# Kernel tuning notes

Measured on AMD Instinct MI355X. Metric: run time of the kernel, lower is better.

## Reference

```python
import jax, jax.numpy as jnp
import numpy as np

B, L, D, C = 32, 2048, 1024, 1024  # batch, max_length, input_size, context_size


def setup_inputs() -> dict:
    key = jax.random.key(0)
    ks = jax.random.split(key, 4)
    sequence = jax.random.normal(ks[0], (B, L, D), dtype=jnp.float32)
    query = jax.random.normal(ks[1], (B, C), dtype=jnp.float32)
    # lengths in [1, L] so every row has at least one unmasked position
    lengths = jax.random.randint(ks[2], (B,), 1, L + 1, dtype=jnp.int32)
    W_h = jax.random.normal(ks[3], (C, D), dtype=jnp.float32) / np.sqrt(D).astype(np.float32)
    b_h = jnp.zeros((C,), dtype=jnp.float32)
    return {"sequence": sequence, "query": query, "lengths": lengths, "W_h": W_h, "b_h": b_h}


def reference(sequence, query, lengths, W_h, b_h):
    # method='general': energies = (W_h @ sequence + b_h) . query
    h = jnp.einsum('bld,cd->blc', sequence, W_h) + b_h          # [B, L, C]
    energies = jnp.einsum('blc,bc->bl', h, query)                # [B, L]
    # sequence_mask(lengths, L): True where position < length
    mask = jnp.arange(energies.shape[1]) < lengths[:, None]      # [B, L]
    # masked_normalization_inf: fill masked positions with -inf, softmax
    masked = jnp.where(mask, energies, -jnp.inf)
    scores = jax.nn.softmax(masked, axis=-1)                     # [B, L]
    contexts = jnp.einsum('bl,bld->bd', scores, sequence)        # [B, D]
    return contexts, scores
```

## Files before the change

### kernel.cpp

```cpp
#include <hip/hip_runtime.h>
#include <math.h>

#define B_ 32
#define L_ 2048
#define D_ 1024
#define C_ 1024
#define WROWS 8
#define BROWS 32
#define NCH (L_ / BROWS)


__global__ __launch_bounds__(256) void k_vpart(const float* __restrict__ q,
                                               const float* __restrict__ W,
                                               float* __restrict__ vpart) {
    int cc = blockIdx.x, dc = blockIdx.y;
    int t  = threadIdx.x;
    __shared__ float qs[B_][65];
    #pragma unroll
    for (int i = 0; i < 8; ++i) {
        int idx = t + i * 256;
        int b = idx >> 6, cl = idx & 63;
        qs[b][cl] = q[b * C_ + cc * 64 + cl];
    }
    __syncthreads();

    int dl4 = t & 15;
    int bg  = t >> 4;
    float4 a0 = {0,0,0,0}, a1 = {0,0,0,0};
    const float4* W4 = reinterpret_cast<const float4*>(W);
    for (int c = 0; c < 64; ++c) {
        float4 w = W4[(size_t)(cc * 64 + c) * (D_ / 4) + dc * 16 + dl4];
        float q0 = qs[bg * 2 + 0][c];
        float q1 = qs[bg * 2 + 1][c];
        a0.x = fmaf(q0, w.x, a0.x); a0.y = fmaf(q0, w.y, a0.y);
        a0.z = fmaf(q0, w.z, a0.z); a0.w = fmaf(q0, w.w, a0.w);
        a1.x = fmaf(q1, w.x, a1.x); a1.y = fmaf(q1, w.y, a1.y);
        a1.z = fmaf(q1, w.z, a1.z); a1.w = fmaf(q1, w.w, a1.w);
    }
    size_t base = ((size_t)cc * B_ + bg * 2) * D_ + dc * 64 + dl4 * 4;
    *reinterpret_cast<float4*>(vpart + base)       = a0;
    *reinterpret_cast<float4*>(vpart + base + D_)  = a1;
}

__global__ __launch_bounds__(256) void k_vreduce(const float* __restrict__ vpart,
                                                 float* __restrict__ v,
                                                 const float* __restrict__ q,
                                                 const float* __restrict__ bh,
                                                 float* __restrict__ cb) {
    int b = blockIdx.x, dq = blockIdx.y, t = threadIdx.x;
    int d = dq * 256 + t;
    float a = 0.f;
    #pragma unroll
    for (int cc = 0; cc < 16; ++cc)
        a += vpart[((size_t)cc * B_ + b) * D_ + d];
    v[(size_t)b * D_ + d] = a;

    if (dq == 0) {
        float s = 0.f;
        for (int c = t; c < C_; c += 256) s += bh[c] * q[b * C_ + c];
        __shared__ float red[256];
        red[t] = s; __syncthreads();
        for (int off = 128; off > 0; off >>= 1) {
            if (t < off) red[t] += red[t + off];
            __syncthreads();
        }
        if (t == 0) cb[b] = red[0];
    }
}

__global__ __launch_bounds__(256) void k_fused(const float* __restrict__ seq,
                                               const float* __restrict__ v,
                                               const float* __restrict__ cb,
                                               const int* __restrict__ lenp,
                                               float* __restrict__ energ,
                                               float* __restrict__ pm,
                                               float* __restrict__ ps,
                                               float* __restrict__ pc) {
    int b  = blockIdx.y;
    int ch = blockIdx.x;
    int len = lenp[b];
    int l0 = ch * BROWS;
    if (l0 >= len) return;
    int wid = threadIdx.x >> 6, lane = threadIdx.x & 63;
    int t = threadIdx.x;
    int lw0 = l0 + wid * WROWS;

    const float* vb = v + (size_t)b * D_;
    float4 v0 = *reinterpret_cast<const float4*>(vb +       lane * 4);
    float4 v1 = *reinterpret_cast<const float4*>(vb + 256 + lane * 4);
    float4 v2 = *reinterpret_cast<const float4*>(vb + 512 + lane * 4);
    float4 v3 = *reinterpret_cast<const float4*>(vb + 768 + lane * 4);
    float cbb = cb[b];

    float m = -INFINITY, s = 0.f;
    float c[16];
    #pragma unroll
    for (int i = 0; i < 16; ++i) c[i] = 0.f;

    __shared__ float e_sm[BROWS];
    __shared__ float lm[4], ls[4];
    __shared__ float lc[4][D_];

    if (lw0 < len) {
        #pragma unroll
        for (int r = 0; r < WROWS; ++r) {
            int l = lw0 + r;
            bool valid = l < len;
            const float* row = seq + ((size_t)b * L_ + l) * D_;
            float4 s0 = *reinterpret_cast<const float4*>(row +       lane * 4);
            float4 s1 = *reinterpret_cast<const float4*>(row + 256 + lane * 4);
            float4 s2 = *reinterpret_cast<const float4*>(row + 512 + lane * 4);
            float4 s3 = *reinterpret_cast<const float4*>(row + 768 + lane * 4);
            float acc = 0.f;
            acc = fmaf(s0.x, v0.x, acc); acc = fmaf(s0.y, v0.y, acc);
            acc = fmaf(s0.z, v0.z, acc); acc = fmaf(s0.w, v0.w, acc);
            acc = fmaf(s1.x, v1.x, acc); acc = fmaf(s1.y, v1.y, acc);
            acc = fmaf(s1.z, v1.z, acc); acc = fmaf(s1.w, v1.w, acc);
            acc = fmaf(s2.x, v2.x, acc); acc = fmaf(s2.y, v2.y, acc);
            acc = fmaf(s2.z, v2.z, acc); acc = fmaf(s2.w, v2.w, acc);
            acc = fmaf(s3.x, v3.x, acc); acc = fmaf(s3.y, v3.y, acc);
            acc = fmaf(s3.z, v3.z, acc); acc = fmaf(s3.w, v3.w, acc);
            #pragma unroll
            for (int off = 32; off; off >>= 1) acc += __shfl_xor(acc, off);
            float e = acc + cbb;
            if (lane == 0) e_sm[wid * WROWS + r] = e;
            float mnew  = valid ? fmaxf(m, e) : m;
            float scale = (m == mnew) ? 1.f : __expf(m - mnew);
            float p     = valid ? __expf(e - mnew) : 0.f;
            s = s * scale + p;
            c[ 0] = fmaf(p, s0.x, c[ 0] * scale); c[ 1] = fmaf(p, s0.y, c[ 1] * scale);
            c[ 2] = fmaf(p, s0.z, c[ 2] * scale); c[ 3] = fmaf(p, s0.w, c[ 3] * scale);
            c[ 4] = fmaf(p, s1.x, c[ 4] * scale); c[ 5] = fmaf(p, s1.y, c[ 5] * scale);
            c[ 6] = fmaf(p, s1.z, c[ 6] * scale); c[ 7] = fmaf(p, s1.w, c[ 7] * scale);
            c[ 8] = fmaf(p, s2.x, c[ 8] * scale); c[ 9] = fmaf(p, s2.y, c[ 9] * scale);
            c[10] = fmaf(p, s2.z, c[10] * scale); c[11] = fmaf(p, s2.w, c[11] * scale);
            c[12] = fmaf(p, s3.x, c[12] * scale); c[13] = fmaf(p, s3.y, c[13] * scale);
            c[14] = fmaf(p, s3.z, c[14] * scale); c[15] = fmaf(p, s3.w, c[15] * scale);
            m = mnew;
        }
    }

    {
        float4 w0 = {c[ 0], c[ 1], c[ 2], c[ 3]};
        float4 w1 = {c[ 4], c[ 5], c[ 6], c[ 7]};
        float4 w2 = {c[ 8], c[ 9], c[10], c[11]};
        float4 w3 = {c[12], c[13], c[14], c[15]};
        *reinterpret_cast<float4*>(&lc[wid][      lane * 4]) = w0;
        *reinterpret_cast<float4*>(&lc[wid][256 + lane * 4]) = w1;
        *reinterpret_cast<float4*>(&lc[wid][512 + lane * 4]) = w2;
        *reinterpret_cast<float4*>(&lc[wid][768 + lane * 4]) = w3;
        if (lane == 0) { lm[wid] = m; ls[wid] = s; }
    }
    __syncthreads();

    if (t < BROWS) energ[(size_t)b * L_ + l0 + t] = e_sm[t];

    float mb = fmaxf(fmaxf(lm[0], lm[1]), fmaxf(lm[2], lm[3]));
    float w0 = (lm[0] == mb) ? 1.f : __expf(lm[0] - mb);
    float w1 = (lm[1] == mb) ? 1.f : __expf(lm[1] - mb);
    float w2 = (lm[2] == mb) ? 1.f : __expf(lm[2] - mb);
    float w3 = (lm[3] == mb) ? 1.f : __expf(lm[3] - mb);
    float sb = w0 * ls[0] + w1 * ls[1] + w2 * ls[2] + w3 * ls[3];

    float4 a0 = *reinterpret_cast<const float4*>(&lc[0][t * 4]);
    float4 a1 = *reinterpret_cast<const float4*>(&lc[1][t * 4]);
    float4 a2 = *reinterpret_cast<const float4*>(&lc[2][t * 4]);
    float4 a3 = *reinterpret_cast<const float4*>(&lc[3][t * 4]);
    float4 o;
    o.x = w0 * a0.x + w1 * a1.x + w2 * a2.x + w3 * a3.x;
    o.y = w0 * a0.y + w1 * a1.y + w2 * a2.y + w3 * a3.y;
    o.z = w0 * a0.z + w1 * a1.z + w2 * a2.z + w3 * a3.z;
    o.w = w0 * a0.w + w1 * a1.w + w2 * a2.w + w3 * a3.w;

    size_t pidx = (size_t)b * NCH + ch;
    if (t == 0) { pm[pidx] = mb; ps[pidx] = sb; }
    *reinterpret_cast<float4*>(pc + pidx * D_ + t * 4) = o;
}

__global__ __launch_bounds__(256) void k_final(const float* __restrict__ pm,
                                               const float* __restrict__ ps,
                                               const float* __restrict__ pc,
                                               const float* __restrict__ energ,
                                               const int* __restrict__ lenp,
                                               float* __restrict__ ctx,
                                               float* __restrict__ scores) {
    int b = blockIdx.x, sl = blockIdx.y, t = threadIdx.x;
    int len = lenp[b];
    int nch = (len + BROWS - 1) / BROWS;
    __shared__ float wgt[NCH];
    __shared__ float Msh, Ssh;
    if (t < 64) {
        float mi = (t < nch) ? pm[(size_t)b * NCH + t] : -INFINITY;
        float si = (t < nch) ? ps[(size_t)b * NCH + t] : 0.f;
        float M = mi;
        #pragma unroll
        for (int off = 32; off; off >>= 1) M = fmaxf(M, __shfl_xor(M, off));
        float ew = (t < nch) ? __expf(mi - M) : 0.f;
        float S  = ew * si;
        #pragma unroll
        for (int off = 32; off; off >>= 1) S += __shfl_xor(S, off);
        if (t < nch) wgt[t] = ew / S;
        if (t == 0) { Msh = M; Ssh = S; }
    }
    __syncthreads();
    float M = Msh;
    float invS = 1.f / Ssh;

    if (t < 128) {
        int d = sl * 128 + t;
        float o = 0.f;
        for (int ch = 0; ch < nch; ++ch)
            o = fmaf(wgt[ch], pc[((size_t)b * NCH + ch) * D_ + d], o);
        ctx[(size_t)b * D_ + d] = o;
    }

    int l = sl * 256 + t;
    float e = energ[(size_t)b * L_ + l];
    scores[(size_t)b * L_ + l] = (l < len) ? __expf(e - M) * invS : 0.f;
}

extern "C" void kernel_launch(void* const* d_in, const int* in_sizes, int n_in,
                              void* d_out, int out_size, void* d_ws, size_t ws_size,
                              hipStream_t stream) {
    const float* seq     = (const float*)d_in[0];
    const float* query   = (const float*)d_in[1];
    const int*   lengths = (const int*)  d_in[2];
    const float* W_h     = (const float*)d_in[3];
    const float* b_h     = (const float*)d_in[4];

    float* out    = (float*)d_out;
    float* ctx    = out;
    float* scores = out + B_ * D_;

    float* ws    = (float*)d_ws;
    float* v     = ws;
    float* cb    = ws + 32768;
    float* energ = ws + 32800;
    float* vpart = ws + 98336;
    float* pm    = ws + 622624;
    float* ps    = ws + 624672;
    float* pc    = ws + 626720;

    k_vpart  <<<dim3(16, 16), 256, 0, stream>>>(query, W_h, vpart);
    k_vreduce<<<dim3(B_, 4), 256, 0, stream>>>(vpart, v, query, b_h, cb);
    k_fused  <<<dim3(NCH, B_), 256, 0, stream>>>(seq, v, cb, lengths, energ, pm, ps, pc);
    k_final  <<<dim3(B_, 8), 256, 0, stream>>>(pm, ps, pc, energ, lengths, ctx, scores);
}
```

Before: 46.86 us.

## Merge four kernels into two using last-block atomic counters for reductions

```diff
diff --git a/kernel.cpp b/kernel.cpp
--- a/kernel.cpp
+++ b/kernel.cpp
@@ -10,12 +10,17 @@
 #define NCH (L_ / BROWS)
 
 
-__global__ __launch_bounds__(256) void k_vpart(const float* __restrict__ q,
-                                               const float* __restrict__ W,
-                                               float* __restrict__ vpart) {
+__global__ __launch_bounds__(256) void k_prep(const float* __restrict__ q,
+                                              const float* __restrict__ W,
+                                              const float* __restrict__ bh,
+                                              float* __restrict__ vpart,
+                                              float* __restrict__ v,
+                                              float* __restrict__ cb,
+                                              int* __restrict__ cnt) {
     int cc = blockIdx.x, dc = blockIdx.y;
     int t  = threadIdx.x;
     __shared__ float qs[B_][65];
+    __shared__ int lastf;
     #pragma unroll
     for (int i = 0; i < 8; ++i) {
         int idx = t + i * 256;
@@ -38,157 +43,164 @@
         a1.z = fmaf(q1, w.z, a1.z); a1.w = fmaf(q1, w.w, a1.w);
     }
     size_t base = ((size_t)cc * B_ + bg * 2) * D_ + dc * 64 + dl4 * 4;
-    *reinterpret_cast<float4*>(vpart + base)       = a0;
-    *reinterpret_cast<float4*>(vpart + base + D_)  = a1;
+    *reinterpret_cast<float4*>(vpart + base)      = a0;
+    *reinterpret_cast<float4*>(vpart + base + D_) = a1;
+
+    __syncthreads();
+    if (t == 0) {
+        __threadfence();
+        int old = atomicAdd(&cnt[dc], 1);
+        lastf = (old == 15);
+    }
+    __syncthreads();
+    if (!lastf) return;
+    __threadfence();
+
+    #pragma unroll
+    for (int i = 0; i < 8; ++i) {
+        int idx = t + i * 256;
+        int b = idx >> 6, dl = idx & 63;
+        int d = dc * 64 + dl;
+        float a = 0.f;
+        #pragma unroll
+        for (int c2 = 0; c2 < 16; ++c2)
+            a += vpart[((size_t)c2 * B_ + b) * D_ + d];
+        v[(size_t)b * D_ + d] = a;
+    }
+    if (dc == 0) {
+        int b = t >> 3, l8 = t & 7;
+        float s = 0.f;
+        for (int c = l8; c < C_; c += 8) s += bh[c] * q[b * C_ + c];
+        s += __shfl_xor(s, 4); s += __shfl_xor(s, 2); s += __shfl_xor(s, 1);
+        if (l8 == 0) cb[b] = s;
+    }
 }
 
-__global__ __launch_bounds__(256) void k_vreduce(const float* __restrict__ vpart,
-                                                 float* __restrict__ v,
-                                                 const float* __restrict__ q,
-                                                 const float* __restrict__ bh,
-                                                 float* __restrict__ cb) {
-    int b = blockIdx.x, dq = blockIdx.y, t = threadIdx.x;
-    int d = dq * 256 + t;
-    float a = 0.f;
-    #pragma unroll
-    for (int cc = 0; cc < 16; ++cc)
-        a += vpart[((size_t)cc * B_ + b) * D_ + d];
-    v[(size_t)b * D_ + d] = a;
-
-    if (dq == 0) {
-        float s = 0.f;
-        for (int c = t; c < C_; c += 256) s += bh[c] * q[b * C_ + c];
-        __shared__ float red[256];
-        red[t] = s; __syncthreads();
-        for (int off = 128; off > 0; off >>= 1) {
-            if (t < off) red[t] += red[t + off];
-            __syncthreads();
-        }
-        if (t == 0) cb[b] = red[0];
-    }
-}
-
-__global__ __launch_bounds__(256) void k_fused(const float* __restrict__ seq,
-                                               const float* __restrict__ v,
-                                               const float* __restrict__ cb,
-                                               const int* __restrict__ lenp,
-                                               float* __restrict__ energ,
-                                               float* __restrict__ pm,
-                                               float* __restrict__ ps,
-                                               float* __restrict__ pc) {
+__global__ __launch_bounds__(256) void k_mega(const float* __restrict__ seq,
+                                              const float* __restrict__ v,
+                                              const float* __restrict__ cb,
+                                              const int* __restrict__ lenp,
+                                              float* __restrict__ energ,
+                                              float* __restrict__ pm,
+                                              float* __restrict__ ps,
+                                              float* __restrict__ pc,
+                                              int* __restrict__ done,
+                                              float* __restrict__ ctx,
+                                              float* __restrict__ scores) {
     int b  = blockIdx.y;
     int ch = blockIdx.x;
     int len = lenp[b];
     int l0 = ch * BROWS;
-    if (l0 >= len) return;
-    int wid = threadIdx.x >> 6, lane = threadIdx.x & 63;
-    int t = threadIdx.x;
-    int lw0 = l0 + wid * WROWS;
-
-    const float* vb = v + (size_t)b * D_;
-    float4 v0 = *reinterpret_cast<const float4*>(vb +       lane * 4);
-    float4 v1 = *reinterpret_cast<const float4*>(vb + 256 + lane * 4);
-    float4 v2 = *reinterpret_cast<const float4*>(vb + 512 + lane * 4);
-    float4 v3 = *reinterpret_cast<const float4*>(vb + 768 + lane * 4);
-    float cbb = cb[b];
-
-    float m = -INFINITY, s = 0.f;
-    float c[16];
-    #pragma unroll
-    for (int i = 0; i < 16; ++i) c[i] = 0.f;
+    int t = threadIdx.x, wid = t >> 6, lane = t & 63;
 
     __shared__ float e_sm[BROWS];
     __shared__ float lm[4], ls[4];
     __shared__ float lc[4][D_];
-
-    if (lw0 < len) {
-        #pragma unroll
-        for (int r = 0; r < WROWS; ++r) {
-            int l = lw0 + r;
-            bool valid = l < len;
-            const float* row = seq + ((size_t)b * L_ + l) * D_;
-            float4 s0 = *reinterpret_cast<const float4*>(row +       lane * 4);
-            float4 s1 = *reinterpret_cast<const float4*>(row + 256 + lane * 4);
-            float4 s2 = *reinterpret_cast<const float4*>(row + 512 + lane * 4);
-            float4 s3 = *reinterpret_cast<const float4*>(row + 768 + lane * 4);
-            float acc = 0.f;
-            acc = fmaf(s0.x, v0.x, acc); acc = fmaf(s0.y, v0.y, acc);
-            acc = fmaf(s0.z, v0.z, acc); acc = fmaf(s0.w, v0.w, acc);
-            acc = fmaf(s1.x, v1.x, acc); acc = fmaf(s1.y, v1.y, acc);
-            acc = fmaf(s1.z, v1.z, acc); acc = fmaf(s1.w, v1.w, acc);
-            acc = fmaf(s2.x, v2.x, acc); acc = fmaf(s2.y, v2.y, acc);
-            acc = fmaf(s2.z, v2.z, acc); acc = fmaf(s2.w, v2.w, acc);
-            acc = fmaf(s3.x, v3.x, acc); acc = fmaf(s3.y, v3.y, acc);
-            acc = fmaf(s3.z, v3.z, acc); acc = fmaf(s3.w, v3.w, acc);
-            #pragma unroll
-            for (int off = 32; off; off >>= 1) acc += __shfl_xor(acc, off);
-            float e = acc + cbb;
-            if (lane == 0) e_sm[wid * WROWS + r] = e;
-            float mnew  = valid ? fmaxf(m, e) : m;
-            float scale = (m == mnew) ? 1.f : __expf(m - mnew);
-            float p     = valid ? __expf(e - mnew) : 0.f;
-            s = s * scale + p;
-            c[ 0] = fmaf(p, s0.x, c[ 0] * scale); c[ 1] = fmaf(p, s0.y, c[ 1] * scale);
-            c[ 2] = fmaf(p, s0.z, c[ 2] * scale); c[ 3] = fmaf(p, s0.w, c[ 3] * scale);
-            c[ 4] = fmaf(p, s1.x, c[ 4] * scale); c[ 5] = fmaf(p, s1.y, c[ 5] * scale);
-            c[ 6] = fmaf(p, s1.z, c[ 6] * scale); c[ 7] = fmaf(p, s1.w, c[ 7] * scale);
-            c[ 8] = fmaf(p, s2.x, c[ 8] * scale); c[ 9] = fmaf(p, s2.y, c[ 9] * scale);
-            c[10] = fmaf(p, s2.z, c[10] * scale); c[11] = fmaf(p, s2.w, c[11] * scale);
-            c[12] = fmaf(p, s3.x, c[12] * scale); c[13] = fmaf(p, s3.y, c[13] * scale);
-            c[14] = fmaf(p, s3.z, c[14] * scale); c[15] = fmaf(p, s3.w, c[15] * scale);
-            m = mnew;
-        }
-    }
-
-    {
-        float4 w0 = {c[ 0], c[ 1], c[ 2], c[ 3]};
-        float4 w1 = {c[ 4], c[ 5], c[ 6], c[ 7]};
-        float4 w2 = {c[ 8], c[ 9], c[10], c[11]};
-        float4 w3 = {c[12], c[13], c[14], c[15]};
-        *reinterpret_cast<float4*>(&lc[wid][      lane * 4]) = w0;
-        *reinterpret_cast<float4*>(&lc[wid][256 + lane * 4]) = w1;
-        *reinterpret_cast<float4*>(&lc[wid][512 + lane * 4]) = w2;
-        *reinterpret_cast<float4*>(&lc[wid][768 + lane * 4]) = w3;
-        if (lane == 0) { lm[wid] = m; ls[wid] = s; }
-    }
-    __syncthreads();
-
-    if (t < BROWS) energ[(size_t)b * L_ + l0 + t] = e_sm[t];
-
-    float mb = fmaxf(fmaxf(lm[0], lm[1]), fmaxf(lm[2], lm[3]));
-    float w0 = (lm[0] == mb) ? 1.f : __expf(lm[0] - mb);
-    float w1 = (lm[1] == mb) ? 1.f : __expf(lm[1] - mb);
-    float w2 = (lm[2] == mb) ? 1.f : __expf(lm[2] - mb);
-    float w3 = (lm[3] == mb) ? 1.f : __expf(lm[3] - mb);
-    float sb = w0 * ls[0] + w1 * ls[1] + w2 * ls[2] + w3 * ls[3];
-
-    float4 a0 = *reinterpret_cast<const float4*>(&lc[0][t * 4]);
-    float4 a1 = *reinterpret_cast<const float4*>(&lc[1][t * 4]);
-    float4 a2 = *reinterpret_cast<const float4*>(&lc[2][t * 4]);
-    float4 a3 = *reinterpret_cast<const float4*>(&lc[3][t * 4]);
-    float4 o;
-    o.x = w0 * a0.x + w1 * a1.x + w2 * a2.x + w3 * a3.x;
-    o.y = w0 * a0.y + w1 * a1.y + w2 * a2.y + w3 * a3.y;
-    o.z = w0 * a0.z + w1 * a1.z + w2 * a2.z + w3 * a3.z;
-    o.w = w0 * a0.w + w1 * a1.w + w2 * a2.w + w3 * a3.w;
-
-    size_t pidx = (size_t)b * NCH + ch;
-    if (t == 0) { pm[pidx] = mb; ps[pidx] = sb; }
-    *reinterpret_cast<float4*>(pc + pidx * D_ + t * 4) = o;
-}
-
-__global__ __launch_bounds__(256) void k_final(const float* __restrict__ pm,
-                                               const float* __restrict__ ps,
-                                               const float* __restrict__ pc,
-                                               const float* __restrict__ energ,
-                                               const int* __restrict__ lenp,
-                                               float* __restrict__ ctx,
-                                               float* __restrict__ scores) {
-    int b = blockIdx.x, sl = blockIdx.y, t = threadIdx.x;
-    int len = lenp[b];
-    int nch = (len + BROWS - 1) / BROWS;
     __shared__ float wgt[NCH];
     __shared__ float Msh, Ssh;
+    __shared__ int lastf;
+
+    if (l0 < len) {
+        int lw0 = l0 + wid * WROWS;
+        const float* vb = v + (size_t)b * D_;
+        float4 v0 = *reinterpret_cast<const float4*>(vb +       lane * 4);
+        float4 v1 = *reinterpret_cast<const float4*>(vb + 256 + lane * 4);
+        float4 v2 = *reinterpret_cast<const float4*>(vb + 512 + lane * 4);
+        float4 v3 = *reinterpret_cast<const float4*>(vb + 768 + lane * 4);
+        float cbb = cb[b];
+
+        float m = -INFINITY, s = 0.f;
+        float c[16];
+        #pragma unroll
+        for (int i = 0; i < 16; ++i) c[i] = 0.f;
+
+        if (lw0 < len) {
+            #pragma unroll
+            for (int r = 0; r < WROWS; ++r) {
+                int l = lw0 + r;
+                bool valid = l < len;
+                const float* row = seq + ((size_t)b * L_ + l) * D_;
+                float4 s0 = *reinterpret_cast<const float4*>(row +       lane * 4);
+                float4 s1 = *reinterpret_cast<const float4*>(row + 256 + lane * 4);
+                float4 s2 = *reinterpret_cast<const float4*>(row + 512 + lane * 4);
+                float4 s3 = *reinterpret_cast<const float4*>(row + 768 + lane * 4);
+                float acc = 0.f;
+                acc = fmaf(s0.x, v0.x, acc); acc = fmaf(s0.y, v0.y, acc);
+                acc = fmaf(s0.z, v0.z, acc); acc = fmaf(s0.w, v0.w, acc);
+                acc = fmaf(s1.x, v1.x, acc); acc = fmaf(s1.y, v1.y, acc);
+                acc = fmaf(s1.z, v1.z, acc); acc = fmaf(s1.w, v1.w, acc);
+                acc = fmaf(s2.x, v2.x, acc); acc = fmaf(s2.y, v2.y, acc);
+                acc = fmaf(s2.z, v2.z, acc); acc = fmaf(s2.w, v2.w, acc);
+                acc = fmaf(s3.x, v3.x, acc); acc = fmaf(s3.y, v3.y, acc);
+                acc = fmaf(s3.z, v3.z, acc); acc = fmaf(s3.w, v3.w, acc);
+                #pragma unroll
+                for (int off = 32; off; off >>= 1) acc += __shfl_xor(acc, off);
+                float e = acc + cbb;
+                if (lane == 0) e_sm[wid * WROWS + r] = e;
+                float mnew  = valid ? fmaxf(m, e) : m;
+                float scale = (m == mnew) ? 1.f : __expf(m - mnew);
+                float p     = valid ? __expf(e - mnew) : 0.f;
+                s = s * scale + p;
+                c[ 0] = fmaf(p, s0.x, c[ 0] * scale); c[ 1] = fmaf(p, s0.y, c[ 1] * scale);
+                c[ 2] = fmaf(p, s0.z, c[ 2] * scale); c[ 3] = fmaf(p, s0.w, c[ 3] * scale);
+                c[ 4] = fmaf(p, s1.x, c[ 4] * scale); c[ 5] = fmaf(p, s1.y, c[ 5] * scale);
+                c[ 6] = fmaf(p, s1.z, c[ 6] * scale); c[ 7] = fmaf(p, s1.w, c[ 7] * scale);
+                c[ 8] = fmaf(p, s2.x, c[ 8] * scale); c[ 9] = fmaf(p, s2.y, c[ 9] * scale);
+                c[10] = fmaf(p, s2.z, c[10] * scale); c[11] = fmaf(p, s2.w, c[11] * scale);
+                c[12] = fmaf(p, s3.x, c[12] * scale); c[13] = fmaf(p, s3.y, c[13] * scale);
+                c[14] = fmaf(p, s3.z, c[14] * scale); c[15] = fmaf(p, s3.w, c[15] * scale);
+                m = mnew;
+            }
+        }
+
+        {
+            float4 w0 = {c[ 0], c[ 1], c[ 2], c[ 3]};
+            float4 w1 = {c[ 4], c[ 5], c[ 6], c[ 7]};
+            float4 w2 = {c[ 8], c[ 9], c[10], c[11]};
+            float4 w3 = {c[12], c[13], c[14], c[15]};
+            *reinterpret_cast<float4*>(&lc[wid][      lane * 4]) = w0;
+            *reinterpret_cast<float4*>(&lc[wid][256 + lane * 4]) = w1;
+            *reinterpret_cast<float4*>(&lc[wid][512 + lane * 4]) = w2;
+            *reinterpret_cast<float4*>(&lc[wid][768 + lane * 4]) = w3;
+            if (lane == 0) { lm[wid] = m; ls[wid] = s; }
+        }
+        __syncthreads();
+
+        if (t < BROWS) energ[(size_t)b * L_ + l0 + t] = e_sm[t];
+
+        float mb = fmaxf(fmaxf(lm[0], lm[1]), fmaxf(lm[2], lm[3]));
+        float w0 = (lm[0] == mb) ? 1.f : __expf(lm[0] - mb);
+        float w1 = (lm[1] == mb) ? 1.f : __expf(lm[1] - mb);
+        float w2 = (lm[2] == mb) ? 1.f : __expf(lm[2] - mb);
+        float w3 = (lm[3] == mb) ? 1.f : __expf(lm[3] - mb);
+        float sb = w0 * ls[0] + w1 * ls[1] + w2 * ls[2] + w3 * ls[3];
+
+        float4 a0 = *reinterpret_cast<const float4*>(&lc[0][t * 4]);
+        float4 a1 = *reinterpret_cast<const float4*>(&lc[1][t * 4]);
+        float4 a2 = *reinterpret_cast<const float4*>(&lc[2][t * 4]);
+        float4 a3 = *reinterpret_cast<const float4*>(&lc[3][t * 4]);
+        float4 o;
+        o.x = w0 * a0.x + w1 * a1.x + w2 * a2.x + w3 * a3.x;
+        o.y = w0 * a0.y + w1 * a1.y + w2 * a2.y + w3 * a3.y;
+        o.z = w0 * a0.z + w1 * a1.z + w2 * a2.z + w3 * a3.z;
+        o.w = w0 * a0.w + w1 * a1.w + w2 * a2.w + w3 * a3.w;
+
+        size_t pidx = (size_t)b * NCH + ch;
+        if (t == 0) { pm[pidx] = mb; ps[pidx] = sb; }
+        *reinterpret_cast<float4*>(pc + pidx * D_ + t * 4) = o;
+        __syncthreads();
+    }
+
+    if (t == 0) {
+        __threadfence();
+        int old = atomicAdd(&done[b], 1);
+        lastf = (old == NCH - 1);
+    }
+    __syncthreads();
+    if (!lastf) return;
+    __threadfence();
+
+    int nch = (len + BROWS - 1) / BROWS;
     if (t < 64) {
         float mi = (t < nch) ? pm[(size_t)b * NCH + t] : -INFINITY;
         float si = (t < nch) ? ps[(size_t)b * NCH + t] : 0.f;
@@ -203,20 +215,22 @@
         if (t == 0) { Msh = M; Ssh = S; }
     }
     __syncthreads();
-    float M = Msh;
-    float invS = 1.f / Ssh;
-
-    if (t < 128) {
-        int d = sl * 128 + t;
+    float M = Msh, invS = 1.f / Ssh;
+
+    #pragma unroll
+    for (int i = 0; i < 4; ++i) {
+        int d = t + i * 256;
         float o = 0.f;
-        for (int ch = 0; ch < nch; ++ch)
-            o = fmaf(wgt[ch], pc[((size_t)b * NCH + ch) * D_ + d], o);
+        for (int c2 = 0; c2 < nch; ++c2)
+            o = fmaf(wgt[c2], pc[((size_t)b * NCH + c2) * D_ + d], o);
         ctx[(size_t)b * D_ + d] = o;
     }
-
-    int l = sl * 256 + t;
-    float e = energ[(size_t)b * L_ + l];
-    scores[(size_t)b * L_ + l] = (l < len) ? __expf(e - M) * invS : 0.f;
+    #pragma unroll
+    for (int i = 0; i < 8; ++i) {
+        int l = t + i * 256;
+        float e = energ[(size_t)b * L_ + l];
+        scores[(size_t)b * L_ + l] = (l < len) ? __expf(e - M) * invS : 0.f;
+    }
 }
 
 extern "C" void kernel_launch(void* const* d_in, const int* in_sizes, int n_in,
@@ -240,9 +254,11 @@
     float* pm    = ws + 622624;
     float* ps    = ws + 624672;
     float* pc    = ws + 626720;
-
-    k_vpart  <<<dim3(16, 16), 256, 0, stream>>>(query, W_h, vpart);
-    k_vreduce<<<dim3(B_, 4), 256, 0, stream>>>(vpart, v, query, b_h, cb);
-    k_fused  <<<dim3(NCH, B_), 256, 0, stream>>>(seq, v, cb, lengths, energ, pm, ps, pc);
-    k_final  <<<dim3(B_, 8), 256, 0, stream>>>(pm, ps, pc, energ, lengths, ctx, scores);
+    int*   cnt   = (int*)(ws + 2723872);
+    int*   done  = cnt + 16;
+
+    hipMemsetAsync(cnt, 0, 48 * sizeof(int), stream);
+    k_prep<<<dim3(16, 16), 256, 0, stream>>>(query, W_h, b_h, vpart, v, cb, cnt);
+    k_mega<<<dim3(NCH, B_), 256, 0, stream>>>(seq, v, cb, lengths, energ, pm, ps, pc,
+                                              done, ctx, scores);
 }
```

New measurement: 160.4 us. 3.42x slower.

## Merge split-K projection and reduction into a single full-K v kernel

Applied to the files above, without the earlier changes.

```diff
diff --git a/kernel.cpp b/kernel.cpp
--- a/kernel.cpp
+++ b/kernel.cpp
@@ -10,61 +10,39 @@
 #define NCH (L_ / BROWS)
 
 
-__global__ __launch_bounds__(256) void k_vpart(const float* __restrict__ q,
-                                               const float* __restrict__ W,
-                                               float* __restrict__ vpart) {
-    int cc = blockIdx.x, dc = blockIdx.y;
+__global__ __launch_bounds__(256) void k_v(const float* __restrict__ q,
+                                           const float* __restrict__ W,
+                                           const float* __restrict__ bh,
+                                           float* __restrict__ v,
+                                           float* __restrict__ cb) {
+    int dc = blockIdx.x;
+    int bg = blockIdx.y;
     int t  = threadIdx.x;
-    __shared__ float qs[B_][65];
+    __shared__ float qs[4][C_];
     #pragma unroll
-    for (int i = 0; i < 8; ++i) {
+    for (int i = 0; i < 4; ++i) {
         int idx = t + i * 256;
-        int b = idx >> 6, cl = idx & 63;
-        qs[b][cl] = q[b * C_ + cc * 64 + cl];
+        int bl = idx >> 8, c4 = idx & 255;
+        *reinterpret_cast<float4*>(&qs[bl][c4 * 4]) =
+            *reinterpret_cast<const float4*>(q + (size_t)(bg * 4 + bl) * C_ + c4 * 4);
     }
     __syncthreads();
 
-    int dl4 = t & 15;
-    int bg  = t >> 4;
-    float4 a0 = {0,0,0,0}, a1 = {0,0,0,0};
-    const float4* W4 = reinterpret_cast<const float4*>(W);
-    for (int c = 0; c < 64; ++c) {
-        float4 w = W4[(size_t)(cc * 64 + c) * (D_ / 4) + dc * 16 + dl4];
-        float q0 = qs[bg * 2 + 0][c];
-        float q1 = qs[bg * 2 + 1][c];
-        a0.x = fmaf(q0, w.x, a0.x); a0.y = fmaf(q0, w.y, a0.y);
-        a0.z = fmaf(q0, w.z, a0.z); a0.w = fmaf(q0, w.w, a0.w);
-        a1.x = fmaf(q1, w.x, a1.x); a1.y = fmaf(q1, w.y, a1.y);
-        a1.z = fmaf(q1, w.z, a1.z); a1.w = fmaf(q1, w.w, a1.w);
-    }
-    size_t base = ((size_t)cc * B_ + bg * 2) * D_ + dc * 64 + dl4 * 4;
-    *reinterpret_cast<float4*>(vpart + base)       = a0;
-    *reinterpret_cast<float4*>(vpart + base + D_)  = a1;
-}
-
-__global__ __launch_bounds__(256) void k_vreduce(const float* __restrict__ vpart,
-                                                 float* __restrict__ v,
-                                                 const float* __restrict__ q,
-                                                 const float* __restrict__ bh,
-                                                 float* __restrict__ cb) {
-    int b = blockIdx.x, dq = blockIdx.y, t = threadIdx.x;
-    int d = dq * 256 + t;
-    float a = 0.f;
-    #pragma unroll
-    for (int cc = 0; cc < 16; ++cc)
-        a += vpart[((size_t)cc * B_ + b) * D_ + d];
-    v[(size_t)b * D_ + d] = a;
-
-    if (dq == 0) {
+    int dl = t & 63, bl = t >> 6;
+    int d = dc * 64 + dl;
+    float a0 = 0.f, a1 = 0.f;
+    for (int c = 0; c < C_; c += 2) {
+        a0 = fmaf(qs[bl][c],     W[(size_t)c * D_ + d],        a0);
+        a1 = fmaf(qs[bl][c + 1], W[(size_t)(c + 1) * D_ + d],  a1);
+    }
+    v[(size_t)(bg * 4 + bl) * D_ + d] = a0 + a1;
+
+    if (dc == 0) {
         float s = 0.f;
-        for (int c = t; c < C_; c += 256) s += bh[c] * q[b * C_ + c];
-        __shared__ float red[256];
-        red[t] = s; __syncthreads();
-        for (int off = 128; off > 0; off >>= 1) {
-            if (t < off) red[t] += red[t + off];
-            __syncthreads();
-        }
-        if (t == 0) cb[b] = red[0];
+        for (int c = dl; c < C_; c += 64) s = fmaf(bh[c], qs[bl][c], s);
+        #pragma unroll
+        for (int off = 32; off; off >>= 1) s += __shfl_xor(s, off);
+        if (dl == 0) cb[bg * 4 + bl] = s;
     }
 }
 
@@ -236,13 +214,11 @@
     float* v     = ws;
     float* cb    = ws + 32768;
     float* energ = ws + 32800;
-    float* vpart = ws + 98336;
     float* pm    = ws + 622624;
     float* ps    = ws + 624672;
     float* pc    = ws + 626720;
 
-    k_vpart  <<<dim3(16, 16), 256, 0, stream>>>(query, W_h, vpart);
-    k_vreduce<<<dim3(B_, 4), 256, 0, stream>>>(vpart, v, query, b_h, cb);
-    k_fused  <<<dim3(NCH, B_), 256, 0, stream>>>(seq, v, cb, lengths, energ, pm, ps, pc);
-    k_final  <<<dim3(B_, 8), 256, 0, stream>>>(pm, ps, pc, energ, lengths, ctx, scores);
-}
+    k_v    <<<dim3(16, 8), 256, 0, stream>>>(query, W_h, b_h, v, cb);
+    k_fused<<<dim3(NCH, B_), 256, 0, stream>>>(seq, v, cb, lengths, energ, pm, ps, pc);
+    k_final<<<dim3(B_, 8), 256, 0, stream>>>(pm, ps, pc, energ, lengths, ctx, scores);
+}
```

New measurement: 68.81 us. +46.8%, slower.
